# Kernel tuning notes

Measured on AMD Instinct MI355X. Metric: run time of the kernel, lower is better.

Reference implementation:

```python
import jax, jax.numpy as jnp
import numpy as np

INF8 = 255
H, D = 8, 64  # num_heads, head dim (hidden=512)
G = 1         # num_global_node


def setup_inputs() -> dict:
    key = jax.random.key(0)
    ks = jax.random.split(key, 12)
    B, N, HID = 8, 1023, 512
    S = N + G
    inp = {
        'q': jax.random.normal(ks[0], (B, S, HID), jnp.float32),
        'k': jax.random.normal(ks[1], (B, S, HID), jnp.float32),
        'v': jax.random.normal(ks[2], (B, S, HID), jnp.float32),
        'attn_bias': jax.random.randint(ks[3], (B, N, N, 1), 0, 255).astype(jnp.int32),
        'Wq': 0.02 * jax.random.normal(ks[4], (HID, HID), jnp.float32),
        'bq': jnp.zeros((HID,), jnp.float32),
        'Wk': 0.02 * jax.random.normal(ks[5], (HID, HID), jnp.float32),
        'bk': jnp.zeros((HID,), jnp.float32),
        'Wv': 0.02 * jax.random.normal(ks[6], (HID, HID), jnp.float32),
        'bv': jnp.zeros((HID,), jnp.float32),
        'Wo': 0.02 * jax.random.normal(ks[7], (HID, HID), jnp.float32),
        'bo': jnp.zeros((HID,), jnp.float32),
        'bias_table': 0.02 * jax.random.normal(ks[8], (INF8 + 1, H), jnp.float32),
        'vbias': 0.02 * jax.random.normal(ks[9], (G, H), jnp.float32),
    }
    return inp


def _structural_bias(attn_bias, bias_table, vbias):
    # attn_bias: [B, N, N, 1] int -> [B, H, N+G, N+G] float
    ab = attn_bias[..., 0]                      # [B,N,N]
    B, N, _ = ab.shape
    bias = bias_table[ab]                       # [B,N,N,H]
    mask = ab == INF8
    bias = jnp.where(mask[..., None], -jnp.inf, bias)
    row = jnp.broadcast_to(vbias[None, :, None, :], (B, G, N, bias.shape[-1]))
    bias = jnp.concatenate([bias, row], axis=1)             # [B,N+G,N,H]
    col = jnp.broadcast_to(vbias[None, None, :, :], (B, N + G, G, bias.shape[-1]))
    bias = jnp.concatenate([bias, col], axis=2)             # [B,N+G,N+G,H]
    return bias.transpose(0, 3, 1, 2)                       # [B,H,S,S]


def reference(q, k, v, attn_bias, Wq, bq, Wk, bk, Wv, bv, Wo, bo, bias_table, vbias):
    B, S, HID = q.shape
    scale = D ** -0.5
    qh = (q @ Wq.T + bq).reshape(B, S, H, D)
    kh = (k @ Wk.T + bk).reshape(B, S, H, D)
    vh = (v @ Wv.T + bv).reshape(B, S, H, D)
    scores = jnp.einsum('bshd,bthd->bhst', qh * scale, kh)  # [B,H,S,S]
    scores = scores + _structural_bias(attn_bias, bias_table, vbias)
    p = jax.nn.softmax(scores, axis=-1)
    # dropout is identity in eval mode
    ctx = jnp.einsum('bhst,bthd->bshd', p, vh).reshape(B, S, HID)
    return ctx @ Wo.T + bo
```

## Files before the change

### kernel.cpp

```cpp
#include <hip/hip_runtime.h>
#include <hip/hip_bf16.h>


typedef __attribute__((ext_vector_type(8)))  __bf16 bf16x8;
typedef __attribute__((ext_vector_type(16))) float  f32x16;

__device__ inline f32x16 zero16(){
  f32x16 z;
  #pragma unroll
  for (int i=0;i<16;i++) z[i] = 0.0f;
  return z;
}

__device__ inline unsigned short f2bf(float x){
  unsigned u = __float_as_uint(x);
  u += 0x7fffu + ((u>>16)&1u);
  return (unsigned short)(u>>16);
}
__device__ inline unsigned f2bf_pair(float a, float b){
  unsigned ua = __float_as_uint(a); ua += 0x7fffu + ((ua>>16)&1u);
  unsigned ub = __float_as_uint(b); ub += 0x7fffu + ((ub>>16)&1u);
  return (ua>>16) | (ub & 0xffff0000u);
}
__device__ inline unsigned comb2(unsigned a, unsigned b, float rn){
  const float a0 = __uint_as_float(a<<16), a1 = __uint_as_float(a & 0xffff0000u);
  const float b0 = __uint_as_float(b<<16), b1 = __uint_as_float(b & 0xffff0000u);
  return f2bf_pair((a0+b0)*rn, (a1+b1)*rn);
}

__device__ inline void bar_lgkm(){
  asm volatile("s_waitcnt lgkmcnt(0)" ::: "memory");
  __builtin_amdgcn_s_barrier();
}

__global__ __launch_bounds__(256)
void ab_transpose(const int* ab, unsigned short* abT)
{
  __shared__ int tl[64*65];
  const int k  = blockIdx.x;
  const int b  = k >> 8;
  const int ti = k & 255;
  const int t0 = (ti & 15) << 6, q0 = (ti >> 4) << 6;
  const int c  = threadIdx.x & 63, r0 = threadIdx.x >> 6;
  #pragma unroll
  for (int rp = 0; rp < 16; ++rp){
    const int r = r0 + rp*4;
    const int q = q0 + r, t = t0 + c;
    int v = 256;
    if (q < 1023 && t < 1023) v = ab[((size_t)b*1023 + q)*1023 + t];
    tl[r*65 + c] = v;
  }
  __syncthreads();
  unsigned short* dst = abT + ((size_t)b << 20);
  #pragma unroll
  for (int rp = 0; rp < 16; ++rp){
    const int r = r0 + rp*4;
    dst[(size_t)(t0 + r)*1024 + q0 + c] = (unsigned short)tl[c*65 + r];
  }
}

__global__ __launch_bounds__(256)
void qkv_proj(const float* xq, const float* xk, const float* xv,
              const float* Wq, const float* Wk, const float* Wv,
              const float* bq, const float* bk, const float* bv,
              unsigned short* qh, unsigned short* kh, unsigned short* vht2,
              float scaleq)
{
  __shared__ unsigned short lda[128*40];
  __shared__ unsigned short ldb[128*40];
  const int bid = blockIdx.x;
  const int sel = bid >> 8;
  const int t   = bid & 255;
  const float *RA, *RB, *bias;
  int r0, c0;
  if (sel == 0){ RA = xq; RB = Wq; bias = bq; r0 = (t&63)*128; c0 = (t>>6)*128; }
  else if (sel == 1){ RA = xk; RB = Wk; bias = bk; r0 = (t&63)*128; c0 = (t>>6)*128; }
  else { RA = Wv; RB = xv; bias = bv; r0 = (t&3)*128; c0 = (t>>2)*128; }

  const int tid  = threadIdx.x;
  const int w    = tid>>6, lane = tid&63, lo = lane&31, hi = lane>>5;
  const int wr   = (w>>1)*64, wc = (w&1)*64;
  const int arow = tid>>1, kb = (tid&1)*16;

  f32x16 acc[2][2];
  #pragma unroll
  for (int i=0;i<2;i++)
    #pragma unroll
    for (int j=0;j<2;j++) acc[i][j] = zero16();

  float4 ra[4], rb4[4];
  {
    const float4* p = (const float4*)(RA + (r0+arow)*512 + kb);
    ra[0]=p[0]; ra[1]=p[1]; ra[2]=p[2]; ra[3]=p[3];
    const float4* pq = (const float4*)(RB + (c0+arow)*512 + kb);
    rb4[0]=pq[0]; rb4[1]=pq[1]; rb4[2]=pq[2]; rb4[3]=pq[3];
  }

  for (int ks=0; ks<16; ++ks){
    bar_lgkm();
    {
      uint4 w0, w1;
      w0.x = f2bf_pair(ra[0].x, ra[0].y); w0.y = f2bf_pair(ra[0].z, ra[0].w);
      w0.z = f2bf_pair(ra[1].x, ra[1].y); w0.w = f2bf_pair(ra[1].z, ra[1].w);
      w1.x = f2bf_pair(ra[2].x, ra[2].y); w1.y = f2bf_pair(ra[2].z, ra[2].w);
      w1.z = f2bf_pair(ra[3].x, ra[3].y); w1.w = f2bf_pair(ra[3].z, ra[3].w);
      uint4* pa = (uint4*)&lda[arow*40 + kb];
      pa[0] = w0; pa[1] = w1;
      uint4 v0, v1;
      v0.x = f2bf_pair(rb4[0].x, rb4[0].y); v0.y = f2bf_pair(rb4[0].z, rb4[0].w);
      v0.z = f2bf_pair(rb4[1].x, rb4[1].y); v0.w = f2bf_pair(rb4[1].z, rb4[1].w);
      v1.x = f2bf_pair(rb4[2].x, rb4[2].y); v1.y = f2bf_pair(rb4[2].z, rb4[2].w);
      v1.z = f2bf_pair(rb4[3].x, rb4[3].y); v1.w = f2bf_pair(rb4[3].z, rb4[3].w);
      uint4* pb = (uint4*)&ldb[arow*40 + kb];
      pb[0] = v0; pb[1] = v1;
    }
    if (ks < 15){
      const int k0 = (ks+1)*32;
      const float4* p = (const float4*)(RA + (r0+arow)*512 + k0 + kb);
      ra[0]=p[0]; ra[1]=p[1]; ra[2]=p[2]; ra[3]=p[3];
      const float4* pq = (const float4*)(RB + (c0+arow)*512 + k0 + kb);
      rb4[0]=pq[0]; rb4[1]=pq[1]; rb4[2]=pq[2]; rb4[3]=pq[3];
    }
    bar_lgkm();
    #pragma unroll
    for (int kf=0; kf<2; ++kf){
      bf16x8 af0 = *(const bf16x8*)&lda[(wr+lo)*40    + kf*16 + hi*8];
      bf16x8 af1 = *(const bf16x8*)&lda[(wr+32+lo)*40 + kf*16 + hi*8];
      bf16x8 bg0 = *(const bf16x8*)&ldb[(wc+lo)*40    + kf*16 + hi*8];
      bf16x8 bg1 = *(const bf16x8*)&ldb[(wc+32+lo)*40 + kf*16 + hi*8];
      acc[0][0] = __builtin_amdgcn_mfma_f32_32x32x16_bf16(af0, bg0, acc[0][0], 0,0,0);
      acc[0][1] = __builtin_amdgcn_mfma_f32_32x32x16_bf16(af0, bg1, acc[0][1], 0,0,0);
      acc[1][0] = __builtin_amdgcn_mfma_f32_32x32x16_bf16(af1, bg0, acc[1][0], 0,0,0);
      acc[1][1] = __builtin_amdgcn_mfma_f32_32x32x16_bf16(af1, bg1, acc[1][1], 0,0,0);
    }
  }

  #pragma unroll
  for (int mi=0;mi<2;mi++){
    #pragma unroll
    for (int ni=0;ni<2;ni++){
      #pragma unroll
      for (int r=0;r<16;r++){
        const int rl = wr + mi*32 + (r&3) + 8*(r>>2) + 4*hi;
        const int cl = wc + ni*32 + lo;
        const int rg = r0 + rl, cg = c0 + cl;
        float v = acc[mi][ni][r];
        if (sel == 0){
          v = (v + bias[cg]) * scaleq;
          const int bb = rg>>10, s = rg&1023, h = cg>>6, d = cg&63;
          qh[(((bb*8+h)*1024)+s)*64 + d] = f2bf(v);
        } else if (sel == 1){
          v = v + bias[cg];
          const int bb = rg>>10, s = rg&1023, h = cg>>6, d = cg&63;
          kh[(((bb*8+h)*1024)+s)*64 + d] = f2bf(v);
        } else {
          v = v + bias[rg];
          const int h = rg>>6, d = rg&63, bb = cg>>10, s = cg&1023;
          vht2[(((size_t)(bb*8+h)*32 + (s>>5))*64 + d)*32 + (s&31)] = f2bf(v);
        }
      }
    }
  }
}

__global__ __launch_bounds__(256)
void out_proj(const unsigned short* ctx0, const unsigned short* ctx1,
              const float* lsump, const float* Wo, const float* bo, float* OUT)
{
  __shared__ unsigned short lda[128*40];
  __shared__ unsigned short ldb[128*40];
  const int tid  = threadIdx.x;
  const int r0   = blockIdx.x*128, c0 = blockIdx.y*128;
  const int w    = tid>>6, lane = tid&63, lo = lane&31, hi = lane>>5;
  const int wr   = (w>>1)*64, wc = (w&1)*64;
  const int arow = tid>>1, kb = (tid&1)*16;
  const int rgs  = r0 + arow, bb = rgs>>10, ss = rgs&1023;
  const float* lb0 = lsump + (size_t)(bb*8)*1024 + ss;
  const float* lb1 = lsump + (size_t)((8+bb)*8)*1024 + ss;

  f32x16 acc[2][2];
  #pragma unroll
  for (int i=0;i<2;i++)
    #pragma unroll
    for (int j=0;j<2;j++) acc[i][j] = zero16();

  uint4 ra0[2], ra1[2];
  float4 rb4[4];
  float l0, l1;

  {
    const uint4* p0 = (const uint4*)(ctx0 + rgs*512 + kb);
    ra0[0]=p0[0]; ra0[1]=p0[1];
    const uint4* p1 = (const uint4*)(ctx1 + rgs*512 + kb);
    ra1[0]=p1[0]; ra1[1]=p1[1];
    const int h = kb>>6;
    l0 = lb0[h*1024]; l1 = lb1[h*1024];
    const float4* pq = (const float4*)(Wo + (c0+arow)*512 + kb);
    rb4[0]=pq[0]; rb4[1]=pq[1]; rb4[2]=pq[2]; rb4[3]=pq[3];
  }

  for (int ks=0; ks<16; ++ks){
    bar_lgkm();
    {
      const float rn = __builtin_amdgcn_rcpf(l0 + l1);
      uint4 w0, w1;
      w0.x = comb2(ra0[0].x, ra1[0].x, rn); w0.y = comb2(ra0[0].y, ra1[0].y, rn);
      w0.z = comb2(ra0[0].z, ra1[0].z, rn); w0.w = comb2(ra0[0].w, ra1[0].w, rn);
      w1.x = comb2(ra0[1].x, ra1[1].x, rn); w1.y = comb2(ra0[1].y, ra1[1].y, rn);
      w1.z = comb2(ra0[1].z, ra1[1].z, rn); w1.w = comb2(ra0[1].w, ra1[1].w, rn);
      uint4* pa = (uint4*)&lda[arow*40 + kb];
      pa[0] = w0; pa[1] = w1;
      uint4 v0, v1;
      v0.x = f2bf_pair(rb4[0].x, rb4[0].y); v0.y = f2bf_pair(rb4[0].z, rb4[0].w);
      v0.z = f2bf_pair(rb4[1].x, rb4[1].y); v0.w = f2bf_pair(rb4[1].z, rb4[1].w);
      v1.x = f2bf_pair(rb4[2].x, rb4[2].y); v1.y = f2bf_pair(rb4[2].z, rb4[2].w);
      v1.z = f2bf_pair(rb4[3].x, rb4[3].y); v1.w = f2bf_pair(rb4[3].z, rb4[3].w);
      uint4* pb = (uint4*)&ldb[arow*40 + kb];
      pb[0] = v0; pb[1] = v1;
    }
    if (ks < 15){
      const int k0 = (ks+1)*32;
      const uint4* p0 = (const uint4*)(ctx0 + rgs*512 + k0 + kb);
      ra0[0]=p0[0]; ra0[1]=p0[1];
      const uint4* p1 = (const uint4*)(ctx1 + rgs*512 + k0 + kb);
      ra1[0]=p1[0]; ra1[1]=p1[1];
      const int h = (k0+kb)>>6;
      l0 = lb0[h*1024]; l1 = lb1[h*1024];
      const float4* pq = (const float4*)(Wo + (c0+arow)*512 + k0 + kb);
      rb4[0]=pq[0]; rb4[1]=pq[1]; rb4[2]=pq[2]; rb4[3]=pq[3];
    }
    bar_lgkm();
    #pragma unroll
    for (int kf=0; kf<2; ++kf){
      bf16x8 af0 = *(const bf16x8*)&lda[(wr+lo)*40    + kf*16 + hi*8];
      bf16x8 af1 = *(const bf16x8*)&lda[(wr+32+lo)*40 + kf*16 + hi*8];
      bf16x8 bg0 = *(const bf16x8*)&ldb[(wc+lo)*40    + kf*16 + hi*8];
      bf16x8 bg1 = *(const bf16x8*)&ldb[(wc+32+lo)*40 + kf*16 + hi*8];
      acc[0][0] = __builtin_amdgcn_mfma_f32_32x32x16_bf16(af0, bg0, acc[0][0], 0,0,0);
      acc[0][1] = __builtin_amdgcn_mfma_f32_32x32x16_bf16(af0, bg1, acc[0][1], 0,0,0);
      acc[1][0] = __builtin_amdgcn_mfma_f32_32x32x16_bf16(af1, bg0, acc[1][0], 0,0,0);
      acc[1][1] = __builtin_amdgcn_mfma_f32_32x32x16_bf16(af1, bg1, acc[1][1], 0,0,0);
    }
  }

  #pragma unroll
  for (int mi=0;mi<2;mi++){
    #pragma unroll
    for (int ni=0;ni<2;ni++){
      #pragma unroll
      for (int r=0;r<16;r++){
        const int rl = wr + mi*32 + (r&3) + 8*(r>>2) + 4*hi;
        const int cl = wc + ni*32 + lo;
        const int rg = r0 + rl, cg = c0 + cl;
        OUT[rg*512 + cg] = acc[mi][ni][r] + bo[cg];
      }
    }
  }
}

__global__ __launch_bounds__(256)
void attn_fused(const unsigned short* qh, const unsigned short* kh,
                const unsigned short* vht2, const unsigned short* abT,
                const float* bias_table, const float* vbias,
                unsigned short* ctxp, float* lsump)
{
  __shared__ float tbl[260];
  __shared__ unsigned short kls[2][32*72];
  __shared__ unsigned short vls[2][64*40];
  __shared__ unsigned short abls[2][32*136];

  const int tid = threadIdx.x;
  const int m   = blockIdx.x;
  const int sg  = m >> 7;
  const int c   = m & 127;
  const int h   = c & 7;
  const int ts  = (c >> 3) & 1;
  const int b   = c >> 4;
  const int tb  = ts*512;
  const int q0  = sg*128;

  for (int i = tid; i < 257; i += 256){
    float v;
    if (i < 255)       v = bias_table[i*8 + h];
    else if (i == 255) v = -1.0e30f;
    else               v = vbias[h];
    tbl[i] = v * 1.4426950408889634f;
  }

  const int w = tid>>6, lane = tid&63, lo = lane&31, hi = lane>>5;
  const bool hib = (hi != 0);
  const int s0 = q0 + w*32;

  const unsigned short* qbase  = qh   + (size_t)(b*8+h)*65536;
  const unsigned short* kbase  = kh   + (size_t)(b*8+h)*65536 + (size_t)tb*64;
  const unsigned short* vbase  = vht2 + ((size_t)(b*8+h)*32 + (tb>>5))*2048;
  const unsigned short* abbase = abT  + ((size_t)b<<20) + q0;

  bf16x8 qf[4];
  #pragma unroll
  for (int kf=0; kf<4; ++kf)
    qf[kf] = *(const bf16x8*)&qbase[(s0+lo)*64 + kf*16 + hi*8];

  f32x16 accv[2]; accv[0] = zero16(); accv[1] = zero16();
  float lsum = 0.0f;

  const int kdst = (tid>>3)*72  + (tid&7)*8;
  const int vdst = (tid>>2)*40  + (tid&3)*8;
  const int adst = (tid>>3)*136 + (tid&7)*16;

  uint4 krg, vrg, ar0, ar1;
  krg = *(const uint4*)&kbase[tid*8];
  vrg = *(const uint4*)&vbase[tid*8];
  ar0 = *(const uint4*)&abbase[(size_t)(tb + (tid>>3))*1024 + (tid&7)*16];
  ar1 = *(const uint4*)&abbase[(size_t)(tb + (tid>>3))*1024 + (tid&7)*16 + 8];
  *(uint4*)&kls[0][kdst]    = krg;
  *(uint4*)&vls[0][vdst]    = vrg;
  *(uint4*)&abls[0][adst]   = ar0;
  *(uint4*)&abls[0][adst+8] = ar1;
  krg = *(const uint4*)&kbase[32*64 + tid*8];
  vrg = *(const uint4*)&vbase[2048 + tid*8];
  ar0 = *(const uint4*)&abbase[(size_t)(tb + 32 + (tid>>3))*1024 + (tid&7)*16];
  ar1 = *(const uint4*)&abbase[(size_t)(tb + 32 + (tid>>3))*1024 + (tid&7)*16 + 8];
  bar_lgkm();

  for (int tt=0; tt<512; tt+=32){
    const int cur = (tt>>5) & 1;
    *(uint4*)&kls[cur^1][kdst]    = krg;
    *(uint4*)&vls[cur^1][vdst]    = vrg;
    *(uint4*)&abls[cur^1][adst]   = ar0;
    *(uint4*)&abls[cur^1][adst+8] = ar1;
    {
      const int tn = (tt+64)&511;
      krg = *(const uint4*)&kbase[tn*64 + tid*8];
      vrg = *(const uint4*)&vbase[(tn>>5)*2048 + tid*8];
      ar0 = *(const uint4*)&abbase[(size_t)(tb + tn + (tid>>3))*1024 + (tid&7)*16];
      ar1 = *(const uint4*)&abbase[(size_t)(tb + tn + (tid>>3))*1024 + (tid&7)*16 + 8];
    }

    f32x16 sc = zero16();
    #pragma unroll
    for (int kf=0; kf<4; ++kf){
      bf16x8 kfr = *(const bf16x8*)&kls[cur][lo*72 + kf*16 + hi*8];
      sc = __builtin_amdgcn_mfma_f32_32x32x16_bf16(kfr, qf[kf], sc, 0,0,0);
    }

    unsigned d[4][2];
    float ls = 0.0f;
    #pragma unroll
    for (int g=0; g<4; ++g){
      float p[4];
      #pragma unroll
      for (int u=0; u<4; ++u){
        const int crow = u + 8*g + 4*hi;
        const int idx  = abls[cur][crow*136 + w*32 + lo];
        p[u] = __builtin_amdgcn_exp2f(sc[4*g+u] + tbl[idx]);
        ls  += p[u];
      }
      d[g][0] = f2bf_pair(p[0], p[1]);
      d[g][1] = f2bf_pair(p[2], p[3]);
    }
    lsum += ls;

    unsigned x[4][2];
    #pragma unroll
    for (int g=0; g<4; ++g){
      x[g][0] = __shfl_xor(d[g][0], 32, 64);
      x[g][1] = __shfl_xor(d[g][1], 32, 64);
    }

    #pragma unroll
    for (int c2=0; c2<2; ++c2){
      union { unsigned u[4]; bf16x8 v; } pc;
      pc.u[0] = hib ? x[2*c2+1][0] : d[2*c2][0];
      pc.u[1] = hib ? x[2*c2+1][1] : d[2*c2][1];
      pc.u[2] = hib ? d[2*c2+1][0] : x[2*c2][0];
      pc.u[3] = hib ? d[2*c2+1][1] : x[2*c2][1];
      bf16x8 vf0 = *(const bf16x8*)&vls[cur][(     lo)*40 + c2*16 + hi*8];
      bf16x8 vf1 = *(const bf16x8*)&vls[cur][(32 + lo)*40 + c2*16 + hi*8];
      accv[0] = __builtin_amdgcn_mfma_f32_32x32x16_bf16(pc.v, vf0, accv[0], 0,0,0);
      accv[1] = __builtin_amdgcn_mfma_f32_32x32x16_bf16(pc.v, vf1, accv[1], 0,0,0);
    }
    bar_lgkm();
  }

  lsum += __shfl_xor(lsum, 32, 64);

  unsigned short* cbase = ctxp + (size_t)ts*4194304;
  #pragma unroll
  for (int dc=0; dc<2; ++dc){
    #pragma unroll
    for (int r=0;r<16;r++){
      const int rq = (r&3) + 8*(r>>2) + 4*hi;
      cbase[((size_t)b*1024 + s0 + rq)*512 + h*64 + dc*32 + lo] = f2bf(accv[dc][r]);
    }
  }
  if (hi == 0){
    lsump[((size_t)(ts*8 + b)*8 + h)*1024 + s0 + lo] = lsum;
  }
}

extern "C" void kernel_launch(void* const* d_in, const int* in_sizes, int n_in,
                              void* d_out, int out_size, void* d_ws, size_t ws_size,
                              hipStream_t stream)
{
  const float* q    = (const float*)d_in[0];
  const float* k    = (const float*)d_in[1];
  const float* v    = (const float*)d_in[2];
  const int*   ab   = (const int*)  d_in[3];
  const float* Wq   = (const float*)d_in[4];
  const float* bq   = (const float*)d_in[5];
  const float* Wk   = (const float*)d_in[6];
  const float* bk   = (const float*)d_in[7];
  const float* Wv   = (const float*)d_in[8];
  const float* bv   = (const float*)d_in[9];
  const float* Wo   = (const float*)d_in[10];
  const float* bo   = (const float*)d_in[11];
  const float* btab = (const float*)d_in[12];
  const float* vbia = (const float*)d_in[13];

  char* ws = (char*)d_ws;
  unsigned short* qh   = (unsigned short*)(ws);
  unsigned short* kh   = (unsigned short*)(ws + ((size_t) 8<<20));
  unsigned short* vht2 = (unsigned short*)(ws + ((size_t)16<<20));
  unsigned short* ctxp = (unsigned short*)(ws + ((size_t)24<<20));
  float*          lsmp = (float*)         (ws + ((size_t)40<<20));
  unsigned short* abT  = (unsigned short*)(ws + ((size_t)41<<20));

  const float SCALE_Q = 0.125f * 1.4426950408889634f;

  qkv_proj<<<768, 256, 0, stream>>>(q, k, v, Wq, Wk, Wv, bq, bk, bv,
                                    qh, kh, vht2, SCALE_Q);
  ab_transpose<<<2048, 256, 0, stream>>>(ab, abT);
  attn_fused<<<1024, 256, 0, stream>>>(qh, kh, vht2, abT, btab, vbia,
                                       ctxp, lsmp);
  out_proj<<<dim3(64,4), 256, 0, stream>>>(ctxp, ctxp + (size_t)4194304,
                                           lsmp, Wo, bo, (float*)d_out);
}
```

Baseline: 127.8 us.

## Pre-convert projection inputs to tiled bf16 and double-buffer QKV GEMM LDS

Adds a conv_bf16 kernel that converts the q/k/v activations and the weights to bf16 once, in a tile-contiguous layout. qkv_proj then loads bf16 directly, with half the bytes per load and no per-tile conversion, and stages them through double-buffered LDS, using one barrier per k-step instead of two. In exchange it adds an extra kernel launch and a full fp32 read plus bf16 write and read-back of the activations. Workspace regions alias the ctx and abT buffers, which later kernels overwrite.

```diff
diff --git a/kernel.cpp b/kernel.cpp
--- a/kernel.cpp
+++ b/kernel.cpp
@@ -31,6 +31,44 @@
 __device__ inline void bar_lgkm(){
   asm volatile("s_waitcnt lgkmcnt(0)" ::: "memory");
   __builtin_amdgcn_s_barrier();
+}
+
+__global__ __launch_bounds__(256)
+void conv_bf16(const float* xq, const float* xk, const float* xv,
+               const float* Wq, const float* Wk, const float* Wv,
+               unsigned short* xqb, unsigned short* xkb, unsigned short* xvb,
+               unsigned short* wqb, unsigned short* wkb, unsigned short* wvb)
+{
+  const int bid = blockIdx.x;
+  const float* src; unsigned short* dst; int rt, khalf;
+  if (bid < 384){
+    const int s = bid >> 7, r = bid & 127;
+    src = (s==0) ? xq : (s==1) ? xk : xv;
+    dst = (s==0) ? xqb : (s==1) ? xkb : xvb;
+    rt = r >> 1; khalf = r & 1;
+  } else {
+    const int i = bid - 384;
+    const int s = i >> 3, r = i & 7;
+    src = (s==0) ? Wq : (s==1) ? Wk : Wv;
+    dst = (s==0) ? wqb : (s==1) ? wkb : wvb;
+    rt = r >> 1; khalf = r & 1;
+  }
+  const int tid = threadIdx.x;
+  const int row = tid >> 1, co = (tid & 1) * 16;
+  const float* sp = src + (size_t)(rt*128 + row)*512 + co;
+  unsigned short* dp = dst + (size_t)rt*65536 + (size_t)khalf*32768 + tid*16;
+  #pragma unroll
+  for (int kt = 0; kt < 8; ++kt){
+    const float4* p = (const float4*)(sp + (khalf*8 + kt)*32);
+    float4 a = p[0], b2 = p[1], c2 = p[2], d2 = p[3];
+    uint4 w0, w1;
+    w0.x = f2bf_pair(a.x, a.y);   w0.y = f2bf_pair(a.z, a.w);
+    w0.z = f2bf_pair(b2.x, b2.y); w0.w = f2bf_pair(b2.z, b2.w);
+    w1.x = f2bf_pair(c2.x, c2.y); w1.y = f2bf_pair(c2.z, c2.w);
+    w1.z = f2bf_pair(d2.x, d2.y); w1.w = f2bf_pair(d2.z, d2.w);
+    uint4* o = (uint4*)(dp + (size_t)kt*4096);
+    o[0] = w0; o[1] = w1;
+  }
 }
 
 __global__ __launch_bounds__(256)
@@ -60,27 +98,32 @@
 }
 
 __global__ __launch_bounds__(256)
-void qkv_proj(const float* xq, const float* xk, const float* xv,
-              const float* Wq, const float* Wk, const float* Wv,
+void qkv_proj(const unsigned short* xqb, const unsigned short* xkb,
+              const unsigned short* xvb, const unsigned short* wqb,
+              const unsigned short* wkb, const unsigned short* wvb,
               const float* bq, const float* bk, const float* bv,
               unsigned short* qh, unsigned short* kh, unsigned short* vht2,
               float scaleq)
 {
-  __shared__ unsigned short lda[128*40];
-  __shared__ unsigned short ldb[128*40];
+  __shared__ unsigned short lda[2][128*40];
+  __shared__ unsigned short ldb[2][128*40];
   const int bid = blockIdx.x;
   const int sel = bid >> 8;
   const int t   = bid & 255;
-  const float *RA, *RB, *bias;
-  int r0, c0;
-  if (sel == 0){ RA = xq; RB = Wq; bias = bq; r0 = (t&63)*128; c0 = (t>>6)*128; }
-  else if (sel == 1){ RA = xk; RB = Wk; bias = bk; r0 = (t&63)*128; c0 = (t>>6)*128; }
-  else { RA = Wv; RB = xv; bias = bv; r0 = (t&3)*128; c0 = (t>>2)*128; }
+  const unsigned short *RA, *RB; const float* bias;
+  int rtA, rtB;
+  if (sel == 0){ RA = xqb; RB = wqb; bias = bq; rtA = t&63; rtB = t>>6; }
+  else if (sel == 1){ RA = xkb; RB = wkb; bias = bk; rtA = t&63; rtB = t>>6; }
+  else { RA = wvb; RB = xvb; bias = bv; rtA = t&3; rtB = t>>2; }
+  const int r0 = rtA*128, c0 = rtB*128;
 
   const int tid  = threadIdx.x;
   const int w    = tid>>6, lane = tid&63, lo = lane&31, hi = lane>>5;
   const int wr   = (w>>1)*64, wc = (w&1)*64;
-  const int arow = tid>>1, kb = (tid&1)*16;
+  const int sdst = (tid>>1)*40 + (tid&1)*16;
+
+  const unsigned short* Abase = RA + (size_t)rtA*65536;
+  const unsigned short* Bbase = RB + (size_t)rtB*65536;
 
   f32x16 acc[2][2];
   #pragma unroll
@@ -88,51 +131,38 @@
     #pragma unroll
     for (int j=0;j<2;j++) acc[i][j] = zero16();
 
-  float4 ra[4], rb4[4];
-  {
-    const float4* p = (const float4*)(RA + (r0+arow)*512 + kb);
-    ra[0]=p[0]; ra[1]=p[1]; ra[2]=p[2]; ra[3]=p[3];
-    const float4* pq = (const float4*)(RB + (c0+arow)*512 + kb);
-    rb4[0]=pq[0]; rb4[1]=pq[1]; rb4[2]=pq[2]; rb4[3]=pq[3];
-  }
+  uint4 ra0, ra1, rb0, rb1;
+  ra0 = *(const uint4*)&Abase[tid*16]; ra1 = *(const uint4*)&Abase[tid*16+8];
+  rb0 = *(const uint4*)&Bbase[tid*16]; rb1 = *(const uint4*)&Bbase[tid*16+8];
+  { uint4* pa = (uint4*)&lda[0][sdst]; pa[0]=ra0; pa[1]=ra1;
+    uint4* pb = (uint4*)&ldb[0][sdst]; pb[0]=rb0; pb[1]=rb1; }
+  ra0 = *(const uint4*)&Abase[4096 + tid*16]; ra1 = *(const uint4*)&Abase[4096 + tid*16+8];
+  rb0 = *(const uint4*)&Bbase[4096 + tid*16]; rb1 = *(const uint4*)&Bbase[4096 + tid*16+8];
+  bar_lgkm();
 
   for (int ks=0; ks<16; ++ks){
-    bar_lgkm();
-    {
-      uint4 w0, w1;
-      w0.x = f2bf_pair(ra[0].x, ra[0].y); w0.y = f2bf_pair(ra[0].z, ra[0].w);
-      w0.z = f2bf_pair(ra[1].x, ra[1].y); w0.w = f2bf_pair(ra[1].z, ra[1].w);
-      w1.x = f2bf_pair(ra[2].x, ra[2].y); w1.y = f2bf_pair(ra[2].z, ra[2].w);
-      w1.z = f2bf_pair(ra[3].x, ra[3].y); w1.w = f2bf_pair(ra[3].z, ra[3].w);
-      uint4* pa = (uint4*)&lda[arow*40 + kb];
-      pa[0] = w0; pa[1] = w1;
-      uint4 v0, v1;
-      v0.x = f2bf_pair(rb4[0].x, rb4[0].y); v0.y = f2bf_pair(rb4[0].z, rb4[0].w);
-      v0.z = f2bf_pair(rb4[1].x, rb4[1].y); v0.w = f2bf_pair(rb4[1].z, rb4[1].w);
-      v1.x = f2bf_pair(rb4[2].x, rb4[2].y); v1.y = f2bf_pair(rb4[2].z, rb4[2].w);
-      v1.z = f2bf_pair(rb4[3].x, rb4[3].y); v1.w = f2bf_pair(rb4[3].z, rb4[3].w);
-      uint4* pb = (uint4*)&ldb[arow*40 + kb];
-      pb[0] = v0; pb[1] = v1;
-    }
+    const int cur = ks & 1;
     if (ks < 15){
-      const int k0 = (ks+1)*32;
-      const float4* p = (const float4*)(RA + (r0+arow)*512 + k0 + kb);
-      ra[0]=p[0]; ra[1]=p[1]; ra[2]=p[2]; ra[3]=p[3];
-      const float4* pq = (const float4*)(RB + (c0+arow)*512 + k0 + kb);
-      rb4[0]=pq[0]; rb4[1]=pq[1]; rb4[2]=pq[2]; rb4[3]=pq[3];
-    }
-    bar_lgkm();
+      uint4* pa = (uint4*)&lda[cur^1][sdst]; pa[0]=ra0; pa[1]=ra1;
+      uint4* pb = (uint4*)&ldb[cur^1][sdst]; pb[0]=rb0; pb[1]=rb1;
+    }
+    if (ks < 14){
+      const size_t o = (size_t)(ks+2)*4096 + tid*16;
+      ra0 = *(const uint4*)&Abase[o]; ra1 = *(const uint4*)&Abase[o+8];
+      rb0 = *(const uint4*)&Bbase[o]; rb1 = *(const uint4*)&Bbase[o+8];
+    }
     #pragma unroll
     for (int kf=0; kf<2; ++kf){
-      bf16x8 af0 = *(const bf16x8*)&lda[(wr+lo)*40    + kf*16 + hi*8];
-      bf16x8 af1 = *(const bf16x8*)&lda[(wr+32+lo)*40 + kf*16 + hi*8];
-      bf16x8 bg0 = *(const bf16x8*)&ldb[(wc+lo)*40    + kf*16 + hi*8];
-      bf16x8 bg1 = *(const bf16x8*)&ldb[(wc+32+lo)*40 + kf*16 + hi*8];
+      bf16x8 af0 = *(const bf16x8*)&lda[cur][(wr+lo)*40    + kf*16 + hi*8];
+      bf16x8 af1 = *(const bf16x8*)&lda[cur][(wr+32+lo)*40 + kf*16 + hi*8];
+      bf16x8 bg0 = *(const bf16x8*)&ldb[cur][(wc+lo)*40    + kf*16 + hi*8];
+      bf16x8 bg1 = *(const bf16x8*)&ldb[cur][(wc+32+lo)*40 + kf*16 + hi*8];
       acc[0][0] = __builtin_amdgcn_mfma_f32_32x32x16_bf16(af0, bg0, acc[0][0], 0,0,0);
       acc[0][1] = __builtin_amdgcn_mfma_f32_32x32x16_bf16(af0, bg1, acc[0][1], 0,0,0);
       acc[1][0] = __builtin_amdgcn_mfma_f32_32x32x16_bf16(af1, bg0, acc[1][0], 0,0,0);
       acc[1][1] = __builtin_amdgcn_mfma_f32_32x32x16_bf16(af1, bg1, acc[1][1], 0,0,0);
     }
+    bar_lgkm();
   }
 
   #pragma unroll
@@ -425,11 +455,19 @@
   unsigned short* ctxp = (unsigned short*)(ws + ((size_t)24<<20));
   float*          lsmp = (float*)         (ws + ((size_t)40<<20));
   unsigned short* abT  = (unsigned short*)(ws + ((size_t)41<<20));
+  unsigned short* xqb  = (unsigned short*)(ws + ((size_t)24<<20));
+  unsigned short* xkb  = (unsigned short*)(ws + ((size_t)32<<20));
+  unsigned short* xvb  = (unsigned short*)(ws + ((size_t)41<<20));
+  unsigned short* wqb  = (unsigned short*)(ws + ((size_t)49<<20));
+  unsigned short* wkb  = (unsigned short*)(ws + ((size_t)49<<20) + 524288);
+  unsigned short* wvb  = (unsigned short*)(ws + ((size_t)50<<20));
 
   const float SCALE_Q = 0.125f * 1.4426950408889634f;
 
-  qkv_proj<<<768, 256, 0, stream>>>(q, k, v, Wq, Wk, Wv, bq, bk, bv,
-                                    qh, kh, vht2, SCALE_Q);
+  conv_bf16<<<408, 256, 0, stream>>>(q, k, v, Wq, Wk, Wv,
+                                     xqb, xkb, xvb, wqb, wkb, wvb);
+  qkv_proj<<<768, 256, 0, stream>>>(xqb, xkb, xvb, wqb, wkb, wvb,
+                                    bq, bk, bv, qh, kh, vht2, SCALE_Q);
   ab_transpose<<<2048, 256, 0, stream>>>(ab, abT);
   attn_fused<<<1024, 256, 0, stream>>>(qh, kh, vht2, abT, btab, vbia,
                                        ctxp, lsmp);
```

Result: slower. 132.8 us (+3.9%).
